# Kernel tuning notes

Measured on AMD Instinct MI355X. Metric: run time of the kernel, lower is better.

The kernel has to match this reference:

```python
import jax, jax.numpy as jnp
import numpy as np

WINDOW_SIZE = 5  # hardcoded in module __init__


def local_window_mask(T, dtype=jnp.float32):
    # Faithful to torch code: start from triu(ones, diagonal=1) (value 1.0 for
    # j > i, NOT -inf!), then set entries outside the band |j - i| <= sz to -inf.
    sz = WINDOW_SIZE // 2
    i = jnp.arange(T)[:, None]
    j = jnp.arange(T)[None, :]
    upper = (j > i).astype(dtype)            # triu part contributes +1 bias
    in_band = jnp.abs(j - i) <= sz
    return jnp.where(in_band, upper, jnp.float32(-jnp.inf).astype(dtype))


def setup_inputs() -> dict:
    key = jax.random.key(0)
    kx, kq, kk, kv = jax.random.split(key, 4)
    B, T, C = 4, 4096, 64
    head_size = 64
    s = 1.0 / np.sqrt(C)
    return {
        "x": jax.random.normal(kx, (B, T, C), dtype=jnp.float32),
        "Wq": jax.random.normal(kq, (head_size, C), dtype=jnp.float32) * s,
        "Wk": jax.random.normal(kk, (head_size, C), dtype=jnp.float32) * s,
        "Wv": jax.random.normal(kv, (head_size, C), dtype=jnp.float32) * s,
    }


def reference(x, Wq, Wk, Wv):
    B, T, C = x.shape
    # nn.Linear(d_model, head_size, bias=False): y = x @ W.T
    q = jnp.einsum('btc,hc->bth', x, Wq)
    k = jnp.einsum('btc,hc->bth', x, Wk)
    v = jnp.einsum('btc,hc->bth', x, Wv)
    scale = jnp.asarray(C, x.dtype) ** -0.5   # scale uses input dim C
    scores = jnp.einsum('bth,bsh->bts', q, k) * scale + local_window_mask(T, x.dtype)
    attn = jax.nn.softmax(scores, axis=-1)    # original computes this twice; once suffices (same math)
    op = jnp.einsum('bts,bsh->bth', attn, v)
    return (op, attn)
```

## Files before the change

kernel.cpp:

```cpp
#include <hip/hip_runtime.h>

constexpr int B      = 4;
constexpr int T      = 4096;
constexpr int C      = 64;
constexpr int H      = 64;
constexpr int TILE   = 32;
constexpr int HALO   = 2;
constexpr int HR     = TILE + 2 * HALO;
constexpr int LS     = 68;
constexpr int NT     = 256;
constexpr int NTILES = T / TILE;
constexpr int CBLOCKS = B * NTILES;
constexpr int FBLOCKS = 2048;
constexpr int T4     = T / 4;
constexpr unsigned TOTAL4 = (unsigned)B * (unsigned)T * (unsigned)T4;

__device__ __forceinline__ void compute_mat(float (*__restrict__ dst)[LS],
                                            const float (*__restrict__ sXl)[LS],
                                            const float (*__restrict__ sWl)[LS],
                                            const int rows, const int srcOff,
                                            const int tid)
{
    const int nrt = rows >> 2;
    if (tid < nrt * 8) {
        const int rt = tid >> 3;
        const int h0 = (tid & 7) << 3;
        int r[4];
#pragma unroll
        for (int k = 0; k < 4; ++k) r[k] = rt + k * nrt + srcOff;

        float acc[4][8];
#pragma unroll
        for (int k = 0; k < 4; ++k)
#pragma unroll
            for (int j = 0; j < 8; ++j) acc[k][j] = 0.f;

        for (int c4 = 0; c4 < C; c4 += 4) {
            float xv[4][4];
#pragma unroll
            for (int k = 0; k < 4; ++k)
                *(float4*)&xv[k][0] = *(const float4*)&sXl[r[k]][c4];
#pragma unroll
            for (int cc = 0; cc < 4; ++cc) {
                const float4 wA = *(const float4*)&sWl[c4 + cc][h0];
                const float4 wB = *(const float4*)&sWl[c4 + cc][h0 + 4];
#pragma unroll
                for (int k = 0; k < 4; ++k) {
                    const float xs = xv[k][cc];
                    acc[k][0] = fmaf(xs, wA.x, acc[k][0]);
                    acc[k][1] = fmaf(xs, wA.y, acc[k][1]);
                    acc[k][2] = fmaf(xs, wA.z, acc[k][2]);
                    acc[k][3] = fmaf(xs, wA.w, acc[k][3]);
                    acc[k][4] = fmaf(xs, wB.x, acc[k][4]);
                    acc[k][5] = fmaf(xs, wB.y, acc[k][5]);
                    acc[k][6] = fmaf(xs, wB.z, acc[k][6]);
                    acc[k][7] = fmaf(xs, wB.w, acc[k][7]);
                }
            }
        }
#pragma unroll
        for (int k = 0; k < 4; ++k) {
            const int rr = r[k] - srcOff;
            *(float4*)&dst[rr][h0]     = make_float4(acc[k][0], acc[k][1], acc[k][2], acc[k][3]);
            *(float4*)&dst[rr][h0 + 4] = make_float4(acc[k][4], acc[k][5], acc[k][6], acc[k][7]);
        }
    }
}

__global__ __launch_bounds__(NT, 2)
void sparse_attn_fused(const float* __restrict__ x,
                       const float* __restrict__ Wq,
                       const float* __restrict__ Wk,
                       const float* __restrict__ Wv,
                       float* __restrict__ out)
{
    __shared__ float sX[HR][LS];
    __shared__ float sW[C][LS];
    __shared__ float sQ[TILE][LS];
    __shared__ float sK[HR][LS];
    __shared__ float sV[HR][LS];
    __shared__ float sS[TILE][8];

    const int tid = threadIdx.x;
    const size_t attnBase = (size_t)B * T * H;

    if (blockIdx.x >= CBLOCKS) {
        float4* __restrict__ attn4 = (float4*)(out + attnBase);
        const unsigned base   = (unsigned)(blockIdx.x - CBLOCKS) * NT + tid;
        const unsigned stride = (unsigned)FBLOCKS * NT;
        const float4 z = make_float4(0.f, 0.f, 0.f, 0.f);
        for (unsigned n = base; n < TOTAL4; n += stride) {
            const int c4 = (int)(n & (T4 - 1));
            const int i  = (int)((n >> 10) & (T - 1));
            const int j0 = c4 << 2;
            if (j0 > i + HALO || j0 + 3 < i - HALO) attn4[n] = z;
        }
        return;
    }

    const int b    = blockIdx.x / NTILES;
    const int tile = blockIdx.x % NTILES;
    const int row0 = tile * TILE;
    const float* xb = x + (size_t)b * T * C;

    for (int s = tid; s < HR * (C / 4); s += NT) {
        const int lr = s >> 4;
        const int c4 = (s & 15) << 2;
        const int gr = row0 + lr - HALO;
        float4 v = make_float4(0.f, 0.f, 0.f, 0.f);
        if (gr >= 0 && gr < T) v = *(const float4*)(xb + (size_t)gr * C + c4);
        *(float4*)&sX[lr][c4] = v;
    }
    for (int s = tid; s < C * H; s += NT) sW[s & 63][s >> 6] = Wq[s];
    __syncthreads();

    compute_mat(sQ, sX, sW, TILE, HALO, tid);
    __syncthreads();

    for (int s = tid; s < C * H; s += NT) sW[s & 63][s >> 6] = Wk[s];
    __syncthreads();

    compute_mat(sK, sX, sW, HR, 0, tid);
    __syncthreads();

    if (tid < TILE * 5) {
        const int i  = tid / 5;
        const int dj = tid % 5;
        const int jg = row0 + i - HALO + dj;
        float sc = -__builtin_inff();
        if (jg >= 0 && jg < T) {
            float acc = 0.f;
#pragma unroll
            for (int h4 = 0; h4 < C; h4 += 4) {
                const float4 q = *(const float4*)&sQ[i][h4];
                const float4 k = *(const float4*)&sK[i + dj][h4];
                acc += q.x * k.x + q.y * k.y + q.z * k.z + q.w * k.w;
            }
            sc = acc * 0.125f + (dj > 2 ? 1.0f : 0.0f);
        }
        sS[i][dj] = sc;
    }
    for (int s = tid; s < C * H; s += NT) sW[s & 63][s >> 6] = Wv[s];
    __syncthreads();

    if (tid < TILE) {
        const int i  = tid;
        const int ig = row0 + i;
        float sc[5];
        float m = -__builtin_inff();
#pragma unroll
        for (int d = 0; d < 5; ++d) { sc[d] = sS[i][d]; m = fmaxf(m, sc[d]); }
        float p[5];
        float sum = 0.f;
#pragma unroll
        for (int d = 0; d < 5; ++d) { p[d] = expf(sc[d] - m); sum += p[d]; }
        const float inv = 1.f / sum;
#pragma unroll
        for (int d = 0; d < 5; ++d) sS[i][d] = p[d] * inv;

        float* rowp = out + attnBase + ((size_t)b * T + ig) * T;
        const int cLo = (ig - HALO > 0 ? ig - HALO : 0) >> 2;
        const int cHi = (ig + HALO < T - 1 ? ig + HALO : T - 1) >> 2;
        for (int c = cLo; c <= cHi; ++c) {
            float vv[4];
#pragma unroll
            for (int q = 0; q < 4; ++q) {
                const int d = (c << 2) + q - (ig - HALO);
                vv[q] = (d >= 0 && d < 5) ? sS[i][d] : 0.f;
            }
            *(float4*)(rowp + (c << 2)) = make_float4(vv[0], vv[1], vv[2], vv[3]);
        }
    }
    __syncthreads();

    compute_mat(sV, sX, sW, HR, 0, tid);
    __syncthreads();

    for (int s = tid; s < TILE * H; s += NT) {
        const int h = s & 63;
        const int r = s >> 6;
        float acc = 0.f;
#pragma unroll
        for (int d = 0; d < 5; ++d) acc = fmaf(sS[r][d], sV[r + d][h], acc);
        out[((size_t)b * T + row0 + r) * H + h] = acc;
    }
}

extern "C" void kernel_launch(void* const* d_in, const int* in_sizes, int n_in,
                              void* d_out, int out_size, void* d_ws, size_t ws_size,
                              hipStream_t stream) {
    (void)in_sizes; (void)n_in; (void)d_ws; (void)ws_size; (void)out_size;
    const float* x  = (const float*)d_in[0];
    const float* Wq = (const float*)d_in[1];
    const float* Wk = (const float*)d_in[2];
    const float* Wv = (const float*)d_in[3];
    float* out = (float*)d_out;
    sparse_attn_fused<<<dim3(CBLOCKS + FBLOCKS), dim3(NT), 0, stream>>>(x, Wq, Wk, Wv, out);
}
```

Before: 307.3 us.

## Refactor attention algebra to skip K/V projections and interleave fill blocks

New measurement: 324.1 us. +5.5%, slower.

```diff
diff --git a/kernel.cpp b/kernel.cpp
--- a/kernel.cpp
+++ b/kernel.cpp
@@ -12,62 +12,11 @@
 constexpr int NTILES = T / TILE;
 constexpr int CBLOCKS = B * NTILES;
 constexpr int FBLOCKS = 2048;
+constexpr int GRID    = CBLOCKS + FBLOCKS;
 constexpr int T4     = T / 4;
 constexpr unsigned TOTAL4 = (unsigned)B * (unsigned)T * (unsigned)T4;
 
-__device__ __forceinline__ void compute_mat(float (*__restrict__ dst)[LS],
-                                            const float (*__restrict__ sXl)[LS],
-                                            const float (*__restrict__ sWl)[LS],
-                                            const int rows, const int srcOff,
-                                            const int tid)
-{
-    const int nrt = rows >> 2;
-    if (tid < nrt * 8) {
-        const int rt = tid >> 3;
-        const int h0 = (tid & 7) << 3;
-        int r[4];
-#pragma unroll
-        for (int k = 0; k < 4; ++k) r[k] = rt + k * nrt + srcOff;
-
-        float acc[4][8];
-#pragma unroll
-        for (int k = 0; k < 4; ++k)
-#pragma unroll
-            for (int j = 0; j < 8; ++j) acc[k][j] = 0.f;
-
-        for (int c4 = 0; c4 < C; c4 += 4) {
-            float xv[4][4];
-#pragma unroll
-            for (int k = 0; k < 4; ++k)
-                *(float4*)&xv[k][0] = *(const float4*)&sXl[r[k]][c4];
-#pragma unroll
-            for (int cc = 0; cc < 4; ++cc) {
-                const float4 wA = *(const float4*)&sWl[c4 + cc][h0];
-                const float4 wB = *(const float4*)&sWl[c4 + cc][h0 + 4];
-#pragma unroll
-                for (int k = 0; k < 4; ++k) {
-                    const float xs = xv[k][cc];
-                    acc[k][0] = fmaf(xs, wA.x, acc[k][0]);
-                    acc[k][1] = fmaf(xs, wA.y, acc[k][1]);
-                    acc[k][2] = fmaf(xs, wA.z, acc[k][2]);
-                    acc[k][3] = fmaf(xs, wA.w, acc[k][3]);
-                    acc[k][4] = fmaf(xs, wB.x, acc[k][4]);
-                    acc[k][5] = fmaf(xs, wB.y, acc[k][5]);
-                    acc[k][6] = fmaf(xs, wB.z, acc[k][6]);
-                    acc[k][7] = fmaf(xs, wB.w, acc[k][7]);
-                }
-            }
-        }
-#pragma unroll
-        for (int k = 0; k < 4; ++k) {
-            const int rr = r[k] - srcOff;
-            *(float4*)&dst[rr][h0]     = make_float4(acc[k][0], acc[k][1], acc[k][2], acc[k][3]);
-            *(float4*)&dst[rr][h0 + 4] = make_float4(acc[k][4], acc[k][5], acc[k][6], acc[k][7]);
-        }
-    }
-}
-
-__global__ __launch_bounds__(NT, 2)
+__global__ __launch_bounds__(NT, 4)
 void sparse_attn_fused(const float* __restrict__ x,
                        const float* __restrict__ Wq,
                        const float* __restrict__ Wk,
@@ -76,17 +25,17 @@
 {
     __shared__ float sX[HR][LS];
     __shared__ float sW[C][LS];
-    __shared__ float sQ[TILE][LS];
-    __shared__ float sK[HR][LS];
-    __shared__ float sV[HR][LS];
+    __shared__ float sU[TILE][LS];
     __shared__ float sS[TILE][8];
 
     const int tid = threadIdx.x;
+    const unsigned bid = blockIdx.x;
     const size_t attnBase = (size_t)B * T * H;
 
-    if (blockIdx.x >= CBLOCKS) {
+    if (bid % 5u != 0u) {
+        const unsigned fid = bid - bid / 5u - 1u;
         float4* __restrict__ attn4 = (float4*)(out + attnBase);
-        const unsigned base   = (unsigned)(blockIdx.x - CBLOCKS) * NT + tid;
+        const unsigned base   = fid * NT + tid;
         const unsigned stride = (unsigned)FBLOCKS * NT;
         const float4 z = make_float4(0.f, 0.f, 0.f, 0.f);
         for (unsigned n = base; n < TOTAL4; n += stride) {
@@ -98,8 +47,9 @@
         return;
     }
 
-    const int b    = blockIdx.x / NTILES;
-    const int tile = blockIdx.x % NTILES;
+    const unsigned cid = bid / 5u;
+    const int b    = (int)(cid / NTILES);
+    const int tile = (int)(cid % NTILES);
     const int row0 = tile * TILE;
     const float* xb = x + (size_t)b * T * C;
 
@@ -111,36 +61,64 @@
         if (gr >= 0 && gr < T) v = *(const float4*)(xb + (size_t)gr * C + c4);
         *(float4*)&sX[lr][c4] = v;
     }
-    for (int s = tid; s < C * H; s += NT) sW[s & 63][s >> 6] = Wq[s];
-    __syncthreads();
-
-    compute_mat(sQ, sX, sW, TILE, HALO, tid);
-    __syncthreads();
-
-    for (int s = tid; s < C * H; s += NT) sW[s & 63][s >> 6] = Wk[s];
-    __syncthreads();
-
-    compute_mat(sK, sX, sW, HR, 0, tid);
-    __syncthreads();
-
-    if (tid < TILE * 5) {
-        const int i  = tid / 5;
-        const int dj = tid % 5;
-        const int jg = row0 + i - HALO + dj;
-        float sc = -__builtin_inff();
-        if (jg >= 0 && jg < T) {
-            float acc = 0.f;
-#pragma unroll
-            for (int h4 = 0; h4 < C; h4 += 4) {
-                const float4 q = *(const float4*)&sQ[i][h4];
-                const float4 k = *(const float4*)&sK[i + dj][h4];
-                acc += q.x * k.x + q.y * k.y + q.z * k.z + q.w * k.w;
-            }
-            sc = acc * 0.125f + (dj > 2 ? 1.0f : 0.0f);
-        }
-        sS[i][dj] = sc;
-    }
-    for (int s = tid; s < C * H; s += NT) sW[s & 63][s >> 6] = Wv[s];
+    {
+        const int c   = tid >> 2;
+        const int cp0 = (tid & 3) << 4;
+        float acc[16];
+#pragma unroll
+        for (int j = 0; j < 16; ++j) acc[j] = 0.f;
+#pragma unroll 4
+        for (int h = 0; h < C; ++h) {
+            const float  wq = Wq[h * 64 + c];
+            const float4 k0 = *(const float4*)&Wk[h * 64 + cp0];
+            const float4 k1 = *(const float4*)&Wk[h * 64 + cp0 + 4];
+            const float4 k2 = *(const float4*)&Wk[h * 64 + cp0 + 8];
+            const float4 k3 = *(const float4*)&Wk[h * 64 + cp0 + 12];
+            acc[0]  = fmaf(wq, k0.x, acc[0]);  acc[1]  = fmaf(wq, k0.y, acc[1]);
+            acc[2]  = fmaf(wq, k0.z, acc[2]);  acc[3]  = fmaf(wq, k0.w, acc[3]);
+            acc[4]  = fmaf(wq, k1.x, acc[4]);  acc[5]  = fmaf(wq, k1.y, acc[5]);
+            acc[6]  = fmaf(wq, k1.z, acc[6]);  acc[7]  = fmaf(wq, k1.w, acc[7]);
+            acc[8]  = fmaf(wq, k2.x, acc[8]);  acc[9]  = fmaf(wq, k2.y, acc[9]);
+            acc[10] = fmaf(wq, k2.z, acc[10]); acc[11] = fmaf(wq, k2.w, acc[11]);
+            acc[12] = fmaf(wq, k3.x, acc[12]); acc[13] = fmaf(wq, k3.y, acc[13]);
+            acc[14] = fmaf(wq, k3.z, acc[14]); acc[15] = fmaf(wq, k3.w, acc[15]);
+        }
+#pragma unroll
+        for (int j = 0; j < 4; ++j)
+            *(float4*)&sW[c][cp0 + 4 * j] =
+                make_float4(acc[4*j], acc[4*j+1], acc[4*j+2], acc[4*j+3]);
+    }
+    __syncthreads();
+
+    {
+        const int r0 = tid >> 4;
+        const int h0 = (tid & 15) << 2;
+        float acc[2][4];
+#pragma unroll
+        for (int k = 0; k < 2; ++k)
+#pragma unroll
+            for (int j = 0; j < 4; ++j) acc[k][j] = 0.f;
+        for (int c4 = 0; c4 < C; c4 += 4) {
+            const float4 xa = *(const float4*)&sX[r0 + HALO][c4];
+            const float4 xc = *(const float4*)&sX[r0 + 16 + HALO][c4];
+#pragma unroll
+            for (int cc = 0; cc < 4; ++cc) {
+                const float4 wv = *(const float4*)&sW[c4 + cc][h0];
+                const float xs0 = (&xa.x)[cc];
+                const float xs1 = (&xc.x)[cc];
+                acc[0][0] = fmaf(xs0, wv.x, acc[0][0]);
+                acc[0][1] = fmaf(xs0, wv.y, acc[0][1]);
+                acc[0][2] = fmaf(xs0, wv.z, acc[0][2]);
+                acc[0][3] = fmaf(xs0, wv.w, acc[0][3]);
+                acc[1][0] = fmaf(xs1, wv.x, acc[1][0]);
+                acc[1][1] = fmaf(xs1, wv.y, acc[1][1]);
+                acc[1][2] = fmaf(xs1, wv.z, acc[1][2]);
+                acc[1][3] = fmaf(xs1, wv.w, acc[1][3]);
+            }
+        }
+        *(float4*)&sU[r0][h0]      = make_float4(acc[0][0], acc[0][1], acc[0][2], acc[0][3]);
+        *(float4*)&sU[r0 + 16][h0] = make_float4(acc[1][0], acc[1][1], acc[1][2], acc[1][3]);
+    }
     __syncthreads();
 
     if (tid < TILE) {
@@ -149,7 +127,22 @@
         float sc[5];
         float m = -__builtin_inff();
 #pragma unroll
-        for (int d = 0; d < 5; ++d) { sc[d] = sS[i][d]; m = fmaxf(m, sc[d]); }
+        for (int d = 0; d < 5; ++d) {
+            const int jg = ig - HALO + d;
+            float v = -__builtin_inff();
+            if (jg >= 0 && jg < T) {
+                float a = 0.f;
+#pragma unroll
+                for (int c4 = 0; c4 < C; c4 += 4) {
+                    const float4 u  = *(const float4*)&sU[i][c4];
+                    const float4 xk = *(const float4*)&sX[i + d][c4];
+                    a += u.x * xk.x + u.y * xk.y + u.z * xk.z + u.w * xk.w;
+                }
+                v = a * 0.125f + (d > 2 ? 1.0f : 0.0f);
+            }
+            sc[d] = v;
+            m = fmaxf(m, v);
+        }
         float p[5];
         float sum = 0.f;
 #pragma unroll
@@ -161,28 +154,74 @@
         float* rowp = out + attnBase + ((size_t)b * T + ig) * T;
         const int cLo = (ig - HALO > 0 ? ig - HALO : 0) >> 2;
         const int cHi = (ig + HALO < T - 1 ? ig + HALO : T - 1) >> 2;
-        for (int c = cLo; c <= cHi; ++c) {
+        for (int cch = cLo; cch <= cHi; ++cch) {
             float vv[4];
 #pragma unroll
             for (int q = 0; q < 4; ++q) {
-                const int d = (c << 2) + q - (ig - HALO);
+                const int d = (cch << 2) + q - (ig - HALO);
                 vv[q] = (d >= 0 && d < 5) ? sS[i][d] : 0.f;
             }
-            *(float4*)(rowp + (c << 2)) = make_float4(vv[0], vv[1], vv[2], vv[3]);
-        }
-    }
-    __syncthreads();
-
-    compute_mat(sV, sX, sW, HR, 0, tid);
-    __syncthreads();
-
-    for (int s = tid; s < TILE * H; s += NT) {
-        const int h = s & 63;
-        const int r = s >> 6;
-        float acc = 0.f;
-#pragma unroll
-        for (int d = 0; d < 5; ++d) acc = fmaf(sS[r][d], sV[r + d][h], acc);
-        out[((size_t)b * T + row0 + r) * H + h] = acc;
+            *(float4*)(rowp + (cch << 2)) = make_float4(vv[0], vv[1], vv[2], vv[3]);
+        }
+    }
+    if (tid >= 64) {
+        for (int s = tid - 64; s < C * H; s += NT - 64)
+            sW[s & 63][s >> 6] = Wv[s];
+    }
+    __syncthreads();
+
+    {
+        const int i  = tid >> 3;
+        const int c0 = (tid & 7) << 3;
+        float y[8];
+#pragma unroll
+        for (int j = 0; j < 8; ++j) y[j] = 0.f;
+#pragma unroll
+        for (int d = 0; d < 5; ++d) {
+            const float pd = sS[i][d];
+            const float4 a = *(const float4*)&sX[i + d][c0];
+            const float4 b2 = *(const float4*)&sX[i + d][c0 + 4];
+            y[0] = fmaf(pd, a.x, y[0]);  y[1] = fmaf(pd, a.y, y[1]);
+            y[2] = fmaf(pd, a.z, y[2]);  y[3] = fmaf(pd, a.w, y[3]);
+            y[4] = fmaf(pd, b2.x, y[4]); y[5] = fmaf(pd, b2.y, y[5]);
+            y[6] = fmaf(pd, b2.z, y[6]); y[7] = fmaf(pd, b2.w, y[7]);
+        }
+        *(float4*)&sU[i][c0]     = make_float4(y[0], y[1], y[2], y[3]);
+        *(float4*)&sU[i][c0 + 4] = make_float4(y[4], y[5], y[6], y[7]);
+    }
+    __syncthreads();
+
+    {
+        const int r0 = tid >> 4;
+        const int h0 = (tid & 15) << 2;
+        float acc[2][4];
+#pragma unroll
+        for (int k = 0; k < 2; ++k)
+#pragma unroll
+            for (int j = 0; j < 4; ++j) acc[k][j] = 0.f;
+        for (int c4 = 0; c4 < C; c4 += 4) {
+            const float4 ya = *(const float4*)&sU[r0][c4];
+            const float4 yc = *(const float4*)&sU[r0 + 16][c4];
+#pragma unroll
+            for (int cc = 0; cc < 4; ++cc) {
+                const float4 wv = *(const float4*)&sW[c4 + cc][h0];
+                const float ys0 = (&ya.x)[cc];
+                const float ys1 = (&yc.x)[cc];
+                acc[0][0] = fmaf(ys0, wv.x, acc[0][0]);
+                acc[0][1] = fmaf(ys0, wv.y, acc[0][1]);
+                acc[0][2] = fmaf(ys0, wv.z, acc[0][2]);
+                acc[0][3] = fmaf(ys0, wv.w, acc[0][3]);
+                acc[1][0] = fmaf(ys1, wv.x, acc[1][0]);
+                acc[1][1] = fmaf(ys1, wv.y, acc[1][1]);
+                acc[1][2] = fmaf(ys1, wv.z, acc[1][2]);
+                acc[1][3] = fmaf(ys1, wv.w, acc[1][3]);
+            }
+        }
+        float* o = out + ((size_t)b * T + row0) * H;
+        *(float4*)&o[(size_t)r0 * H + h0] =
+            make_float4(acc[0][0], acc[0][1], acc[0][2], acc[0][3]);
+        *(float4*)&o[(size_t)(r0 + 16) * H + h0] =
+            make_float4(acc[1][0], acc[1][1], acc[1][2], acc[1][3]);
     }
 }
 
@@ -195,5 +234,5 @@
     const float* Wk = (const float*)d_in[2];
     const float* Wv = (const float*)d_in[3];
     float* out = (float*)d_out;
-    sparse_attn_fused<<<dim3(CBLOCKS + FBLOCKS), dim3(NT), 0, stream>>>(x, Wq, Wk, Wv, out);
+    sparse_attn_fused<<<dim3(GRID), dim3(NT), 0, stream>>>(x, Wq, Wk, Wv, out);
 }
```
